# Optimization experiments

Measured on AMD Instinct MI355X. Metric: run time of the kernel, lower is better.

The kernel has to match this reference:

```python
import jax, jax.numpy as jnp
import numpy as np
from jax import lax

WEIGHT = 1.0
NUM_DILATION_STEPS = 20
FAR_DIST = 20.0


def _neighbor_count(x, kernel, num_classes):
    # grouped 3x3 conv with center tap zeroed, SAME padding (stride 1)
    return lax.conv_general_dilated(
        x, kernel, window_strides=(1, 1), padding='SAME',
        feature_group_count=num_classes,
        dimension_numbers=('NCHW', 'OIHW', 'NCHW'))


def fast_sdf(target_mask, num_classes):
    # target_mask: [B, H, W] int labels -> per-class chamfer-ish distance map [B, C, H, W]
    one_hot = jnp.transpose(jax.nn.one_hot(target_mask, num_classes, dtype=jnp.float32),
                            (0, 3, 1, 2))  # [B, C, H, W]
    foreground = (one_hot > 0.5).astype(jnp.float32)

    # 3x3 all-ones kernel with center zero, one per class (grouped conv)
    k = np.ones((num_classes, 1, 3, 3), dtype=np.float32)
    k[:, 0, 1, 1] = 0.0
    kernel = jnp.asarray(k)

    dist_map0 = jnp.zeros_like(foreground)

    def step(i, state):
        dist_map, current_mask = state
        dilated = (_neighbor_count(current_mask, kernel, num_classes) > 0).astype(jnp.float32)
        # note: faithful to torch code -- pixels with no neighbors vanish and
        # contribute negative increments, exactly as `dilated - current_mask` does
        new_pixels = dilated - current_mask
        dist_map = dist_map + new_pixels * (i + 1).astype(jnp.float32)
        return (dist_map, dilated)

    dist_map, current_mask = lax.fori_loop(0, NUM_DILATION_STEPS, step,
                                           (dist_map0, foreground))
    return jnp.where(current_mask == 0, FAR_DIST, dist_map)


def setup_inputs() -> dict:
    key = jax.random.key(0)
    k1, k2 = jax.random.split(key)
    B, C, H, W = 8, 19, 512, 512
    pred = jax.random.normal(k1, (B, C, H, W), dtype=jnp.float32)
    target = jax.random.randint(k2, (B, H, W), 0, C, dtype=jnp.int64)
    return {"pred": pred, "target": target}


def reference(pred, target):
    num_classes = pred.shape[1]
    probs = jax.nn.softmax(pred, axis=1)
    gt_sdf = lax.stop_gradient(fast_sdf(target, num_classes))
    loss = jnp.mean(probs * gt_sdf)
    return WEIGHT * loss
```

## Files before the change

### kernel.cpp

```cpp
#include <hip/hip_runtime.h>

#define B_ 8
#define C_ 19
#define H_ 512
#define W_ 512
#define HW_ (H_*W_)

#define HALO   20
#define SINT   56
#define SROWS  96
#define NSTRIP 10
#define LSTR   9

typedef unsigned long long u64;

__global__ __launch_bounds__(256) void mask_kernel(const int* __restrict__ target,
                                                   u64* __restrict__ masks) {
    __shared__ u64 mlds[64][21];
    const int blk  = blockIdx.x;
    const int b    = blk >> 6;
    const int base = (blk & 63) * 64;
    const int tid  = threadIdx.x;
    const int lane = tid & 63, wv = tid >> 6;
    const int* tgt = target + b * HW_;
    for (int t = 0; t < 16; ++t) {
        const int cl = wv * 16 + t;
        const int x  = tgt[(base + cl) * 64 + lane];
        u64 keep = 0;
        #pragma unroll
        for (int c = 0; c < C_; ++c) {
            u64 m = __ballot(x == c);
            if (lane == c) keep = m;
        }
        if (lane < C_) mlds[cl][lane] = keep;
    }
    __syncthreads();
    for (int idx = tid; idx < C_ * 64; idx += 256) {
        const int c = idx >> 6, wl = idx & 63;
        masks[((size_t)b * C_ + c) * 4096 + base + wl] = mlds[wl][c];
    }
}

__global__ __launch_bounds__(256) void invd_kernel(const float* __restrict__ pred,
                                                   float* __restrict__ invd) {
    const int t   = blockIdx.x * 256 + threadIdx.x;
    const int b   = t >> 16;
    const int hw4 = (t & 65535) << 2;
    const float* pbase = pred + (size_t)b * C_ * HW_ + hw4;
    float s0=0.f, s1=0.f, s2=0.f, s3=0.f;
    #pragma unroll
    for (int c = 0; c < C_; ++c) {
        float4 v = *(const float4*)(pbase + (size_t)c * HW_);
        s0 += __expf(v.x); s1 += __expf(v.y); s2 += __expf(v.z); s3 += __expf(v.w);
    }
    float4 o; o.x = 1.0f/s0; o.y = 1.0f/s1; o.z = 1.0f/s2; o.w = 1.0f/s3;
    *(float4*)(invd + (size_t)b * HW_ + hw4) = o;
}

__global__ __launch_bounds__(256) void sdf_loss_kernel(const u64* __restrict__ masks,
                                                       const float* __restrict__ pred,
                                                       const float* __restrict__ invd,
                                                       float* __restrict__ out) {
    __shared__ u64 bufA[SROWS * LSTR];
    __shared__ u64 bufB[SROWS * LSTR];
    __shared__ int chg[2];
    __shared__ float part[4];
    const int blk   = blockIdx.x;
    const int strip = blk % NSTRIP;
    const int bc    = blk / NSTRIP;
    const int b     = bc / C_;
    const int c     = bc - b * C_;
    const int y0    = strip * SINT;
    const int tid   = threadIdx.x;
    const int w     = tid & 7;
    const int r0    = (tid >> 3) * 3;
    const u64* mk   = masks + ((size_t)b * C_ + c) * 4096;

    if (tid < 2) chg[tid] = 0;

    u64 save[3], hreg[3], iso[3], pl[3][5];
    #pragma unroll
    for (int i = 0; i < 3; ++i) {
        iso[i] = 0;
        #pragma unroll
        for (int j = 0; j < 5; ++j) pl[i][j] = 0;
    }

    #pragma unroll
    for (int i = 0; i < 3; ++i) {
        const int gy = y0 - HALO + r0 + i;
        save[i] = (gy >= 0 && gy < H_) ? mk[gy * 8 + w] : 0;
    }

    u64 nc[3];
    {
        unsigned mp = (unsigned)(save[0] >> 63) | ((unsigned)(save[1] >> 63) << 1) | ((unsigned)(save[2] >> 63) << 2);
        unsigned lp = ((unsigned)save[0] & 1) | (((unsigned)save[1] & 1) << 1) | (((unsigned)save[2] & 1) << 2);
        unsigned fl = __shfl_up(mp, 1);   if (w == 0) fl = 0;
        unsigned fr = __shfl_down(lp, 1); if (w == 7) fr = 0;
        #pragma unroll
        for (int i = 0; i < 3; ++i) {
            nc[i]   = (save[i] << 1) | (save[i] >> 1) | (u64)((fl >> i) & 1) | ((u64)((fr >> i) & 1) << 63);
            hreg[i] = nc[i] | save[i];
            bufA[(r0 + i) * LSTR + w] = hreg[i];
        }
    }
    __syncthreads();

    u64* cur = bufA;
    u64* nxt = bufB;
    bool done = false;

    {
        u64 hup = (r0 > 0)          ? cur[(r0 - 1) * LSTR + w] : 0;
        u64 hdn = (r0 + 3 < SROWS)  ? cur[(r0 + 3) * LSTR + w] : 0;
        u64 nbr[3], d[3];
        nbr[0] = nc[0] | hup     | hreg[1];
        nbr[1] = nc[1] | hreg[0] | hreg[2];
        nbr[2] = nc[2] | hreg[1] | hdn;
        u64 diff = 0;
        #pragma unroll
        for (int i = 0; i < 3; ++i) {
            iso[i] = save[i] & ~nbr[i];
            d[i]   = save[i] | nbr[i];
            u64 nb = d[i] ^ save[i];
            pl[i][0] |= nb;
            diff |= nb;
            save[i] = d[i];
        }
        unsigned mp = (unsigned)(d[0] >> 63) | ((unsigned)(d[1] >> 63) << 1) | ((unsigned)(d[2] >> 63) << 2);
        unsigned lp = ((unsigned)d[0] & 1) | (((unsigned)d[1] & 1) << 1) | (((unsigned)d[2] & 1) << 2);
        unsigned fl = __shfl_up(mp, 1);   if (w == 0) fl = 0;
        unsigned fr = __shfl_down(lp, 1); if (w == 7) fr = 0;
        #pragma unroll
        for (int i = 0; i < 3; ++i) {
            hreg[i] = d[i] | (d[i] << 1) | (d[i] >> 1) | (u64)((fl >> i) & 1) | ((u64)((fr >> i) & 1) << 63);
            nxt[(r0 + i) * LSTR + w] = hreg[i];
        }
        if (diff) chg[1] = 1;
        if (tid == 0) chg[0] = 0;
        __syncthreads();
        if (!chg[1]) done = true;
        else { u64* t = cur; cur = nxt; nxt = t; }
    }

    if (!done) {
        #pragma unroll
        for (int s = 2; s <= 19; ++s) {
            u64 hup = (r0 > 0)         ? cur[(r0 - 1) * LSTR + w] : 0;
            u64 hdn = (r0 + 3 < SROWS) ? cur[(r0 + 3) * LSTR + w] : 0;
            u64 d[3];
            d[0] = hup     | hreg[0] | hreg[1];
            d[1] = hreg[0] | hreg[1] | hreg[2];
            d[2] = hreg[1] | hreg[2] | hdn;
            u64 diff = 0;
            #pragma unroll
            for (int i = 0; i < 3; ++i) {
                u64 nb = d[i] ^ save[i];
                diff |= nb;
                if (s & 1)  pl[i][0] |= nb;
                if (s & 2)  pl[i][1] |= nb;
                if (s & 4)  pl[i][2] |= nb;
                if (s & 8)  pl[i][3] |= nb;
                if (s & 16) pl[i][4] |= nb;
                save[i] = d[i];
            }
            unsigned mp = (unsigned)(d[0] >> 63) | ((unsigned)(d[1] >> 63) << 1) | ((unsigned)(d[2] >> 63) << 2);
            unsigned lp = ((unsigned)d[0] & 1) | (((unsigned)d[1] & 1) << 1) | (((unsigned)d[2] & 1) << 2);
            unsigned fl = __shfl_up(mp, 1);   if (w == 0) fl = 0;
            unsigned fr = __shfl_down(lp, 1); if (w == 7) fr = 0;
            #pragma unroll
            for (int i = 0; i < 3; ++i) {
                hreg[i] = d[i] | (d[i] << 1) | (d[i] >> 1) | (u64)((fl >> i) & 1) | ((u64)((fr >> i) & 1) << 63);
                nxt[(r0 + i) * LSTR + w] = hreg[i];
            }
            if (diff) chg[s & 1] = 1;
            if (tid == 0) chg[(s + 1) & 1] = 0;
            __syncthreads();
            if (!chg[s & 1]) break;
            u64* t = cur; cur = nxt; nxt = t;
        }
    }

    float acc = 0.f;
    #pragma unroll
    for (int i = 0; i < 3; ++i) {
        const int lr = r0 + i;
        const int gy = y0 - HALO + lr;
        if (lr < HALO || lr >= HALO + SINT || gy >= H_) continue;
        pl[i][0] |= iso[i];
        const u64 m = ~save[i];
        pl[i][2] |= m;
        pl[i][4] |= m;
        u64 q[8];
        #pragma unroll
        for (int g = 0; g < 8; ++g) {
            u64 x = 0;
            #pragma unroll
            for (int j = 0; j < 5; ++j)
                x |= ((pl[i][j] >> (8 * g)) & 0xFFULL) << (8 * j);
            u64 t;
            t = (x ^ (x >> 7))  & 0x00AA00AA00AA00AAULL; x ^= t ^ (t << 7);
            t = (x ^ (x >> 14)) & 0x0000CCCC0000CCCCULL; x ^= t ^ (t << 14);
            t = (x ^ (x >> 28)) & 0x00000000F0F0F0F0ULL; x ^= t ^ (t << 28);
            q[g] = x;
        }
        const float4* pp = (const float4*)(pred + ((size_t)b * C_ + c) * HW_ + gy * W_ + w * 64);
        const float4* dd = (const float4*)(invd + (size_t)b * HW_ + gy * W_ + w * 64);
        #pragma unroll
        for (int k = 0; k < 16; ++k) {
            const float4 v  = pp[k];
            const float4 dv = dd[k];
            const u64 qq = q[k >> 1];
            const int sh = (k & 1) * 32;
            acc = fmaf(__expf(v.x) * dv.x, (float)(unsigned)((qq >> (sh     )) & 0xFF), acc);
            acc = fmaf(__expf(v.y) * dv.y, (float)(unsigned)((qq >> (sh +  8)) & 0xFF), acc);
            acc = fmaf(__expf(v.z) * dv.z, (float)(unsigned)((qq >> (sh + 16)) & 0xFF), acc);
            acc = fmaf(__expf(v.w) * dv.w, (float)(unsigned)((qq >> (sh + 24)) & 0xFF), acc);
        }
    }

    #pragma unroll
    for (int off = 32; off > 0; off >>= 1) acc += __shfl_down(acc, off);
    if ((tid & 63) == 0) part[tid >> 6] = acc;
    __syncthreads();
    if (tid == 0) {
        float s = (part[0] + part[1]) + (part[2] + part[3]);
        atomicAdd(out, s * (1.0f / 39845888.0f));
    }
}

extern "C" void kernel_launch(void* const* d_in, const int* in_sizes, int n_in,
                              void* d_out, int out_size, void* d_ws, size_t ws_size,
                              hipStream_t stream) {
    const float* pred   = (const float*)d_in[0];
    const int*   target = (const int*)d_in[1];
    float* invd = (float*)d_ws;
    u64*   masks = (u64*)((char*)d_ws + 8388608);
    float* out = (float*)d_out;

    hipMemsetAsync(out, 0, sizeof(float), stream);
    mask_kernel<<<512, 256, 0, stream>>>(target, masks);
    invd_kernel<<<2048, 256, 0, stream>>>(pred, invd);
    sdf_loss_kernel<<<B_ * C_ * NSTRIP, 256, 0, stream>>>(masks, pred, invd, out);
}
```

Baseline: 298.6 us.

## Fuse softmax denominator into SDF kernel with per-strip all-class dilation in LDS

Removes the separate inverse-denominator kernel and its workspace round trip. Each block now handles one 8-row strip for all 19 classes of one batch image. Each wavefront runs the bit-parallel dilation entirely in registers using cross-lane shuffles and __any instead of LDS buffers and __syncthreads. The per-pixel distance bytes are staged in shared memory, and pred is then read exactly once to compute both the softmax sum and the weighted numerator. The trade-off is far more halo recomputation (48 rows computed for every 8 useful rows), large LDS use per block, and fewer blocks.

```diff
diff --git a/kernel.cpp b/kernel.cpp
--- a/kernel.cpp
+++ b/kernel.cpp
@@ -7,10 +7,9 @@
 #define HW_ (H_*W_)
 
 #define HALO   20
-#define SINT   56
-#define SROWS  96
-#define NSTRIP 10
-#define LSTR   9
+#define INTR   8
+#define WIN    48
+#define NSTRIP 64
 
 typedef unsigned long long u64;
 
@@ -41,183 +40,162 @@
     }
 }
 
-__global__ __launch_bounds__(256) void invd_kernel(const float* __restrict__ pred,
-                                                   float* __restrict__ invd) {
-    const int t   = blockIdx.x * 256 + threadIdx.x;
-    const int b   = t >> 16;
-    const int hw4 = (t & 65535) << 2;
-    const float* pbase = pred + (size_t)b * C_ * HW_ + hw4;
-    float s0=0.f, s1=0.f, s2=0.f, s3=0.f;
-    #pragma unroll
-    for (int c = 0; c < C_; ++c) {
-        float4 v = *(const float4*)(pbase + (size_t)c * HW_);
-        s0 += __expf(v.x); s1 += __expf(v.y); s2 += __expf(v.z); s3 += __expf(v.w);
-    }
-    float4 o; o.x = 1.0f/s0; o.y = 1.0f/s1; o.z = 1.0f/s2; o.w = 1.0f/s3;
-    *(float4*)(invd + (size_t)b * HW_ + hw4) = o;
-}
-
-__global__ __launch_bounds__(256) void sdf_loss_kernel(const u64* __restrict__ masks,
+__global__ __launch_bounds__(256, 2) void fused_kernel(const u64* __restrict__ masks,
                                                        const float* __restrict__ pred,
-                                                       const float* __restrict__ invd,
                                                        float* __restrict__ out) {
-    __shared__ u64 bufA[SROWS * LSTR];
-    __shared__ u64 bufB[SROWS * LSTR];
-    __shared__ int chg[2];
+    __shared__ unsigned char sdfl[C_ * INTR * W_];
     __shared__ float part[4];
     const int blk   = blockIdx.x;
-    const int strip = blk % NSTRIP;
-    const int bc    = blk / NSTRIP;
-    const int b     = bc / C_;
-    const int c     = bc - b * C_;
-    const int y0    = strip * SINT;
+    const int strip = blk & 63;
+    const int b     = blk >> 6;
     const int tid   = threadIdx.x;
-    const int w     = tid & 7;
-    const int r0    = (tid >> 3) * 3;
-    const u64* mk   = masks + ((size_t)b * C_ + c) * 4096;
-
-    if (tid < 2) chg[tid] = 0;
-
-    u64 save[3], hreg[3], iso[3], pl[3][5];
-    #pragma unroll
-    for (int i = 0; i < 3; ++i) {
-        iso[i] = 0;
-        #pragma unroll
-        for (int j = 0; j < 5; ++j) pl[i][j] = 0;
-    }
-
-    #pragma unroll
-    for (int i = 0; i < 3; ++i) {
-        const int gy = y0 - HALO + r0 + i;
-        save[i] = (gy >= 0 && gy < H_) ? mk[gy * 8 + w] : 0;
-    }
-
-    u64 nc[3];
-    {
-        unsigned mp = (unsigned)(save[0] >> 63) | ((unsigned)(save[1] >> 63) << 1) | ((unsigned)(save[2] >> 63) << 2);
-        unsigned lp = ((unsigned)save[0] & 1) | (((unsigned)save[1] & 1) << 1) | (((unsigned)save[2] & 1) << 2);
-        unsigned fl = __shfl_up(mp, 1);   if (w == 0) fl = 0;
-        unsigned fr = __shfl_down(lp, 1); if (w == 7) fr = 0;
-        #pragma unroll
-        for (int i = 0; i < 3; ++i) {
-            nc[i]   = (save[i] << 1) | (save[i] >> 1) | (u64)((fl >> i) & 1) | ((u64)((fr >> i) & 1) << 63);
-            hreg[i] = nc[i] | save[i];
-            bufA[(r0 + i) * LSTR + w] = hreg[i];
-        }
-    }
-    __syncthreads();
-
-    u64* cur = bufA;
-    u64* nxt = bufB;
-    bool done = false;
-
-    {
-        u64 hup = (r0 > 0)          ? cur[(r0 - 1) * LSTR + w] : 0;
-        u64 hdn = (r0 + 3 < SROWS)  ? cur[(r0 + 3) * LSTR + w] : 0;
-        u64 nbr[3], d[3];
-        nbr[0] = nc[0] | hup     | hreg[1];
-        nbr[1] = nc[1] | hreg[0] | hreg[2];
-        nbr[2] = nc[2] | hreg[1] | hdn;
-        u64 diff = 0;
-        #pragma unroll
-        for (int i = 0; i < 3; ++i) {
-            iso[i] = save[i] & ~nbr[i];
-            d[i]   = save[i] | nbr[i];
-            u64 nb = d[i] ^ save[i];
-            pl[i][0] |= nb;
-            diff |= nb;
-            save[i] = d[i];
-        }
-        unsigned mp = (unsigned)(d[0] >> 63) | ((unsigned)(d[1] >> 63) << 1) | ((unsigned)(d[2] >> 63) << 2);
-        unsigned lp = ((unsigned)d[0] & 1) | (((unsigned)d[1] & 1) << 1) | (((unsigned)d[2] & 1) << 2);
-        unsigned fl = __shfl_up(mp, 1);   if (w == 0) fl = 0;
-        unsigned fr = __shfl_down(lp, 1); if (w == 7) fr = 0;
-        #pragma unroll
-        for (int i = 0; i < 3; ++i) {
-            hreg[i] = d[i] | (d[i] << 1) | (d[i] >> 1) | (u64)((fl >> i) & 1) | ((u64)((fr >> i) & 1) << 63);
-            nxt[(r0 + i) * LSTR + w] = hreg[i];
-        }
-        if (diff) chg[1] = 1;
-        if (tid == 0) chg[0] = 0;
-        __syncthreads();
-        if (!chg[1]) done = true;
-        else { u64* t = cur; cur = nxt; nxt = t; }
-    }
-
-    if (!done) {
-        #pragma unroll
-        for (int s = 2; s <= 19; ++s) {
-            u64 hup = (r0 > 0)         ? cur[(r0 - 1) * LSTR + w] : 0;
-            u64 hdn = (r0 + 3 < SROWS) ? cur[(r0 + 3) * LSTR + w] : 0;
-            u64 d[3];
-            d[0] = hup     | hreg[0] | hreg[1];
-            d[1] = hreg[0] | hreg[1] | hreg[2];
-            d[2] = hreg[1] | hreg[2] | hdn;
-            u64 diff = 0;
-            #pragma unroll
-            for (int i = 0; i < 3; ++i) {
-                u64 nb = d[i] ^ save[i];
-                diff |= nb;
-                if (s & 1)  pl[i][0] |= nb;
-                if (s & 2)  pl[i][1] |= nb;
-                if (s & 4)  pl[i][2] |= nb;
-                if (s & 8)  pl[i][3] |= nb;
-                if (s & 16) pl[i][4] |= nb;
-                save[i] = d[i];
-            }
-            unsigned mp = (unsigned)(d[0] >> 63) | ((unsigned)(d[1] >> 63) << 1) | ((unsigned)(d[2] >> 63) << 2);
-            unsigned lp = ((unsigned)d[0] & 1) | (((unsigned)d[1] & 1) << 1) | (((unsigned)d[2] & 1) << 2);
+    const int wv    = tid >> 6, lane = tid & 63;
+    const int w     = lane & 7, g = lane >> 3;
+    const int gytop = strip * INTR - HALO;
+
+    for (int c = wv; c < C_; c += 4) {
+        const u64* mk = masks + ((size_t)b * C_ + c) * 4096;
+        u64 cov[6], h[6], iso[6], pl[6][5];
+
+        #pragma unroll
+        for (int i = 0; i < 6; ++i) {
+            const int gy = gytop + g * 6 + i;
+            cov[i] = (gy >= 0 && gy < H_) ? mk[gy * 8 + w] : 0;
+            iso[i] = 0;
+            #pragma unroll
+            for (int j = 0; j < 5; ++j) pl[i][j] = 0;
+        }
+
+        u64 nc[6];
+        {
+            unsigned mp = 0, lp = 0;
+            #pragma unroll
+            for (int i = 0; i < 6; ++i) {
+                mp |= (unsigned)(cov[i] >> 63) << i;
+                lp |= ((unsigned)cov[i] & 1) << i;
+            }
             unsigned fl = __shfl_up(mp, 1);   if (w == 0) fl = 0;
             unsigned fr = __shfl_down(lp, 1); if (w == 7) fr = 0;
             #pragma unroll
-            for (int i = 0; i < 3; ++i) {
-                hreg[i] = d[i] | (d[i] << 1) | (d[i] >> 1) | (u64)((fl >> i) & 1) | ((u64)((fr >> i) & 1) << 63);
-                nxt[(r0 + i) * LSTR + w] = hreg[i];
-            }
-            if (diff) chg[s & 1] = 1;
-            if (tid == 0) chg[(s + 1) & 1] = 0;
-            __syncthreads();
-            if (!chg[s & 1]) break;
-            u64* t = cur; cur = nxt; nxt = t;
-        }
-    }
+            for (int i = 0; i < 6; ++i) {
+                nc[i] = (cov[i] << 1) | (cov[i] >> 1) | (u64)((fl >> i) & 1) | ((u64)((fr >> i) & 1) << 63);
+                h[i]  = nc[i] | cov[i];
+            }
+        }
+
+        bool active;
+        {
+            u64 hup = __shfl_up(h[5], 8);   if (g == 0) hup = 0;
+            u64 hdn = __shfl_down(h[0], 8); if (g == 7) hdn = 0;
+            u64 d[6], diffw = 0;
+            #pragma unroll
+            for (int i = 0; i < 6; ++i) {
+                const u64 up  = (i > 0) ? h[i - 1] : hup;
+                const u64 dn  = (i < 5) ? h[i + 1] : hdn;
+                const u64 nbr = nc[i] | up | dn;
+                iso[i] = cov[i] & ~nbr;
+                const u64 nb = nbr & ~cov[i];
+                pl[i][0] = nb;
+                d[i] = cov[i] | nbr;
+                diffw |= nb;
+                cov[i] = d[i];
+            }
+            unsigned mp = 0, lp = 0;
+            #pragma unroll
+            for (int i = 0; i < 6; ++i) {
+                mp |= (unsigned)(cov[i] >> 63) << i;
+                lp |= ((unsigned)cov[i] & 1) << i;
+            }
+            unsigned fl = __shfl_up(mp, 1);   if (w == 0) fl = 0;
+            unsigned fr = __shfl_down(lp, 1); if (w == 7) fr = 0;
+            #pragma unroll
+            for (int i = 0; i < 6; ++i)
+                h[i] = cov[i] | (cov[i] << 1) | (cov[i] >> 1) | (u64)((fl >> i) & 1) | ((u64)((fr >> i) & 1) << 63);
+            active = __any(diffw != 0);
+        }
+
+        if (active) {
+            #pragma unroll
+            for (int s = 2; s <= 19; ++s) {
+                u64 hup = __shfl_up(h[5], 8);   if (g == 0) hup = 0;
+                u64 hdn = __shfl_down(h[0], 8); if (g == 7) hdn = 0;
+                u64 diffw = 0;
+                #pragma unroll
+                for (int i = 0; i < 6; ++i) {
+                    const u64 up = (i > 0) ? h[i - 1] : hup;
+                    const u64 dn = (i < 5) ? h[i + 1] : hdn;
+                    const u64 d  = up | h[i] | dn;
+                    const u64 nb = d ^ cov[i];
+                    diffw |= nb;
+                    if (s & 1)  pl[i][0] |= nb;
+                    if (s & 2)  pl[i][1] |= nb;
+                    if (s & 4)  pl[i][2] |= nb;
+                    if (s & 8)  pl[i][3] |= nb;
+                    if (s & 16) pl[i][4] |= nb;
+                    cov[i] = d;
+                }
+                if (!__any(diffw != 0)) break;
+                if (s < 19) {
+                    unsigned mp = 0, lp = 0;
+                    #pragma unroll
+                    for (int i = 0; i < 6; ++i) {
+                        mp |= (unsigned)(cov[i] >> 63) << i;
+                        lp |= ((unsigned)cov[i] & 1) << i;
+                    }
+                    unsigned fl = __shfl_up(mp, 1);   if (w == 0) fl = 0;
+                    unsigned fr = __shfl_down(lp, 1); if (w == 7) fr = 0;
+                    #pragma unroll
+                    for (int i = 0; i < 6; ++i)
+                        h[i] = cov[i] | (cov[i] << 1) | (cov[i] >> 1) | (u64)((fl >> i) & 1) | ((u64)((fr >> i) & 1) << 63);
+                }
+            }
+        }
+
+        #pragma unroll
+        for (int i = 0; i < 6; ++i) {
+            const int lr = g * 6 + i;
+            if (lr < HALO || lr >= HALO + INTR) continue;
+            pl[i][0] |= iso[i];
+            const u64 m = ~cov[i];
+            pl[i][2] |= m;
+            pl[i][4] |= m;
+            u64* dst = (u64*)&sdfl[(c * INTR + (lr - HALO)) * W_ + w * 64];
+            #pragma unroll
+            for (int g2 = 0; g2 < 8; ++g2) {
+                u64 x = 0;
+                #pragma unroll
+                for (int j = 0; j < 5; ++j)
+                    x |= ((pl[i][j] >> (8 * g2)) & 0xFFULL) << (8 * j);
+                u64 t;
+                t = (x ^ (x >> 7))  & 0x00AA00AA00AA00AAULL; x ^= t ^ (t << 7);
+                t = (x ^ (x >> 14)) & 0x0000CCCC0000CCCCULL; x ^= t ^ (t << 14);
+                t = (x ^ (x >> 28)) & 0x00000000F0F0F0F0ULL; x ^= t ^ (t << 28);
+                dst[g2] = x;
+            }
+        }
+    }
+    __syncthreads();
 
     float acc = 0.f;
+    const float* pb = pred + (size_t)b * C_ * HW_ + (size_t)strip * INTR * W_;
     #pragma unroll
-    for (int i = 0; i < 3; ++i) {
-        const int lr = r0 + i;
-        const int gy = y0 - HALO + lr;
-        if (lr < HALO || lr >= HALO + SINT || gy >= H_) continue;
-        pl[i][0] |= iso[i];
-        const u64 m = ~save[i];
-        pl[i][2] |= m;
-        pl[i][4] |= m;
-        u64 q[8];
-        #pragma unroll
-        for (int g = 0; g < 8; ++g) {
-            u64 x = 0;
-            #pragma unroll
-            for (int j = 0; j < 5; ++j)
-                x |= ((pl[i][j] >> (8 * g)) & 0xFFULL) << (8 * j);
-            u64 t;
-            t = (x ^ (x >> 7))  & 0x00AA00AA00AA00AAULL; x ^= t ^ (t << 7);
-            t = (x ^ (x >> 14)) & 0x0000CCCC0000CCCCULL; x ^= t ^ (t << 14);
-            t = (x ^ (x >> 28)) & 0x00000000F0F0F0F0ULL; x ^= t ^ (t << 28);
-            q[g] = x;
-        }
-        const float4* pp = (const float4*)(pred + ((size_t)b * C_ + c) * HW_ + gy * W_ + w * 64);
-        const float4* dd = (const float4*)(invd + (size_t)b * HW_ + gy * W_ + w * 64);
-        #pragma unroll
-        for (int k = 0; k < 16; ++k) {
-            const float4 v  = pp[k];
-            const float4 dv = dd[k];
-            const u64 qq = q[k >> 1];
-            const int sh = (k & 1) * 32;
-            acc = fmaf(__expf(v.x) * dv.x, (float)(unsigned)((qq >> (sh     )) & 0xFF), acc);
-            acc = fmaf(__expf(v.y) * dv.y, (float)(unsigned)((qq >> (sh +  8)) & 0xFF), acc);
-            acc = fmaf(__expf(v.z) * dv.z, (float)(unsigned)((qq >> (sh + 16)) & 0xFF), acc);
-            acc = fmaf(__expf(v.w) * dv.w, (float)(unsigned)((qq >> (sh + 24)) & 0xFF), acc);
-        }
+    for (int k = 0; k < 4; ++k) {
+        const int p = k * 1024 + tid * 4;
+        float4 den = {0.f, 0.f, 0.f, 0.f};
+        float4 num = {0.f, 0.f, 0.f, 0.f};
+        #pragma unroll
+        for (int c = 0; c < C_; ++c) {
+            const float4 v  = *(const float4*)(pb + (size_t)c * HW_ + p);
+            const uchar4 sv = *(const uchar4*)&sdfl[c * 4096 + p];
+            const float e0 = __expf(v.x), e1 = __expf(v.y);
+            const float e2 = __expf(v.z), e3 = __expf(v.w);
+            den.x += e0; den.y += e1; den.z += e2; den.w += e3;
+            num.x = fmaf(e0, (float)sv.x, num.x);
+            num.y = fmaf(e1, (float)sv.y, num.y);
+            num.z = fmaf(e2, (float)sv.z, num.z);
+            num.w = fmaf(e3, (float)sv.w, num.w);
+        }
+        acc += num.x / den.x + num.y / den.y + num.z / den.z + num.w / den.w;
     }
 
     #pragma unroll
@@ -235,12 +213,10 @@
                               hipStream_t stream) {
     const float* pred   = (const float*)d_in[0];
     const int*   target = (const int*)d_in[1];
-    float* invd = (float*)d_ws;
-    u64*   masks = (u64*)((char*)d_ws + 8388608);
+    u64* masks = (u64*)d_ws;
     float* out = (float*)d_out;
 
     hipMemsetAsync(out, 0, sizeof(float), stream);
     mask_kernel<<<512, 256, 0, stream>>>(target, masks);
-    invd_kernel<<<2048, 256, 0, stream>>>(pred, invd);
-    sdf_loss_kernel<<<B_ * C_ * NSTRIP, 256, 0, stream>>>(masks, pred, invd, out);
+    fused_kernel<<<B_ * NSTRIP, 256, 0, stream>>>(masks, pred, out);
 }
```

Result: faster. 277.4 us (-7.1%).
